# Kernel tuning notes

Hardware: AMD Instinct MI355X
Metric: run time of the kernel (lower is better)

## Reference

```python
import jax, jax.numpy as jnp
import numpy as np

DT = 0.05
TAU = 0.15
SIGMA = float(np.sqrt(2.0 * DT / TAU))  # GaussianNoise default sigma
NOISE_SCALE = 1.0

N = 2048        # nneurons
RANK = 64       # nbg
BATCH = 2048
IN_DIM = 128    # input_sources['stim'] size


def setup_inputs() -> dict:
    key = jax.random.key(0)
    ks = jax.random.split(key, 10)
    inv_sqrt_n = 1.0 / np.sqrt(N)
    return {
        "r_thalamic": jax.random.uniform(ks[0], (BATCH, RANK), jnp.float32),
        "stim": jax.random.normal(ks[1], (BATCH, IN_DIM), jnp.float32),
        "x": jax.random.normal(ks[2], (BATCH, N), jnp.float32) * inv_sqrt_n,
        "r": jax.nn.softplus(jax.random.normal(ks[3], (BATCH, N), jnp.float32) * inv_sqrt_n),
        "J": jax.random.normal(ks[4], (N, N), jnp.float32) * (1.2 * inv_sqrt_n),
        "B": jax.random.normal(ks[5], (1, N), jnp.float32),
        "U": jax.random.normal(ks[6], (N, RANK), jnp.float32) * inv_sqrt_n,
        "V": jax.random.normal(ks[7], (RANK, N), jnp.float32) * inv_sqrt_n,
        "I_stim": jax.random.normal(ks[8], (IN_DIM, N), jnp.float32) * inv_sqrt_n,
        "eps": jax.random.normal(ks[9], (BATCH, N), jnp.float32),
    }


def reference(r_thalamic, stim, x, r, J, B, U, V, I_stim, eps):
    # external input: stim @ I['stim']  -> (batch, N)
    ext = stim @ I_stim
    # bg_tensor @ r == U @ diag(r_thalamic) @ V @ r, computed in low-rank form:
    # (batch, rank) * (batch, rank) -> project back with U
    rec_input = (r_thalamic * (r @ V.T)) @ U.T          # (batch, N)
    pre = -x + r @ J + rec_input + B + ext               # (batch, N)
    noisy = pre + (SIGMA * NOISE_SCALE) * eps            # GaussianNoise
    x_new = x + (DT / TAU) * noisy
    r_new = jax.nn.softplus(x_new)
    return (x_new, r_new)
```

## Files before the change

### kernel.cpp

```cpp
#include <hip/hip_runtime.h>
#include <cstdint>
#include <cstddef>


#define KA 2176
#define KB 2240
#define NN 2048

using frag_ab = __attribute__((ext_vector_type(8))) short;
using frag_cd = __attribute__((ext_vector_type(4))) float;

__device__ __forceinline__ unsigned short f2bf(float f) {
  union { float f; unsigned int i; } v;
  v.f = f;
  unsigned int r = v.i + 0x7fffu + ((v.i >> 16) & 1u);
  return (unsigned short)(r >> 16);
}

__device__ __forceinline__ uint4 cvt8(const float* __restrict__ p) {
  float4 a = *(const float4*)p;
  float4 b = *(const float4*)(p + 4);
  union { uint4 v; unsigned short u[8]; } d;
  d.u[0] = f2bf(a.x); d.u[1] = f2bf(a.y); d.u[2] = f2bf(a.z); d.u[3] = f2bf(a.w);
  d.u[4] = f2bf(b.x); d.u[5] = f2bf(b.y); d.u[6] = f2bf(b.z); d.u[7] = f2bf(b.w);
  return d.v;
}

__device__ __forceinline__ void gl_lds16(const void* g, void* l) {
  __builtin_amdgcn_global_load_lds(
      (const __attribute__((address_space(1))) void*)g,
      (__attribute__((address_space(3))) void*)l, 16, 0, 0);
}

__global__ __launch_bounds__(256) void prep(
    const float* __restrict__ J, const float* __restrict__ Ist,
    const float* __restrict__ rg, const float* __restrict__ stim,
    const float* __restrict__ U, const float* __restrict__ V,
    unsigned short* __restrict__ Ap, unsigned short* __restrict__ Bp,
    float* __restrict__ part) {
  __shared__ unsigned short tile[64 * 66];
  __shared__ alignas(16) unsigned short Ats[32 * 64];
  __shared__ alignas(16) unsigned short Bts[64 * 64];
  const int blk = blockIdx.x;
  const int t = threadIdx.x;

  if (blk < 1088) {
    const float* src;
    int dst_off, cx, cy;
    if (blk < 1024) { src = J;   dst_off = 0;    cx = blk & 31; cy = blk >> 5; }
    else            { src = Ist; dst_off = 2048; cx = (blk - 1024) & 31; cy = (blk - 1024) >> 5; }
    const int r0 = cy * 64, c0 = cx * 64;
    const int sr = t >> 3, c8 = t & 7;
#pragma unroll
    for (int p = 0; p < 2; ++p) {
      const int row = sr + 32 * p;
      union { uint4 v; unsigned short u[8]; } d;
      d.v = cvt8(&src[(size_t)(r0 + row) * 2048 + c0 + c8 * 8]);
#pragma unroll
      for (int e = 0; e < 8; ++e) tile[row * 66 + c8 * 8 + e] = d.u[e];
    }
    __syncthreads();
#pragma unroll
    for (int p = 0; p < 2; ++p) {
      const int scol = sr + 32 * p;
      union { uint4 v; unsigned short u[8]; } d;
#pragma unroll
      for (int e = 0; e < 8; ++e) d.u[e] = tile[(c8 * 8 + e) * 66 + scol];
      *(uint4*)&Bp[(size_t)(c0 + scol) * KB + dst_off + r0 + c8 * 8] = d.v;
    }
  } else if (blk < 3136) {
    const int row = blk - 1088;
    *(uint4*)&Ap[(size_t)row * KA + t * 8] = cvt8(&rg[(size_t)row * 2048 + t * 8]);
    if (t < 24) {
      const int c = 256 + t;
      if (c < 272)
        *(uint4*)&Ap[(size_t)row * KA + c * 8] =
            cvt8(&stim[(size_t)row * 128 + (c - 256) * 8]);
      else
        *(uint4*)&Bp[(size_t)row * KB + c * 8] =
            cvt8(&U[(size_t)row * 64 + (c - 272) * 8]);
    }
  } else {
    const int tb = blk - 3136;
    const int mt = tb & 63, s = tb >> 6;
    const int b0 = mt * 32;
    const int wave = t >> 6, lane = t & 63;
    const int q = lane >> 4, l15 = lane & 15;
    const int arow = t >> 3, ac8 = t & 7;

    const float* gA  = rg + (size_t)(b0 + arow) * 2048 + s * 512 + ac8 * 8;
    const float* gB0 = V  + (size_t)arow        * 2048 + s * 512 + ac8 * 8;
    const float* gB1 = V  + (size_t)(arow + 32) * 2048 + s * 512 + ac8 * 8;

    frag_cd acc0 = {0.f, 0.f, 0.f, 0.f};
    frag_cd acc1 = {0.f, 0.f, 0.f, 0.f};

    for (int kt = 0; kt < 8; ++kt) {
      const int k0 = kt * 64;
      uint4 va  = cvt8(gA + k0);
      uint4 vb0 = cvt8(gB0 + k0);
      uint4 vb1 = cvt8(gB1 + k0);
      __syncthreads();
      *(uint4*)&Ats[t * 8]        = va;
      *(uint4*)&Bts[t * 8]        = vb0;
      *(uint4*)&Bts[2048 + t * 8] = vb1;
      __syncthreads();
#pragma unroll
      for (int ks = 0; ks < 2; ++ks) {
        frag_ab a0 = *(const frag_ab*)&Ats[(l15)      * 64 + ks * 32 + q * 8];
        frag_ab a1 = *(const frag_ab*)&Ats[(16 + l15) * 64 + ks * 32 + q * 8];
        frag_ab b  = *(const frag_ab*)&Bts[(wave * 16 + l15) * 64 + ks * 32 + q * 8];
        acc0 = __builtin_amdgcn_mfma_f32_16x16x32_bf16(a0, b, acc0, 0, 0, 0);
        acc1 = __builtin_amdgcn_mfma_f32_16x16x32_bf16(a1, b, acc1, 0, 0, 0);
      }
    }
    const int p = wave * 16 + l15;
#pragma unroll
    for (int reg = 0; reg < 4; ++reg) {
      const int m0 = q * 4 + reg;
      part[((size_t)s * 2048 + b0 + m0) * 64 + p]      = acc0[reg];
      part[((size_t)s * 2048 + b0 + m0 + 16) * 64 + p] = acc1[reg];
    }
  }
}

__global__ __launch_bounds__(256, 4) void main_gemm(
    const unsigned short* __restrict__ Ap, const unsigned short* __restrict__ Bp,
    const float* __restrict__ part, const float* __restrict__ tha,
    const float* __restrict__ xg, const float* __restrict__ epsg,
    const float* __restrict__ Bvec,
    float* __restrict__ outx, float* __restrict__ outr) {
  __shared__ alignas(16) unsigned short As[64 * 64];
  __shared__ alignas(16) unsigned short Bs[64 * 64];

  const int t = threadIdx.x;
  const int wave = t >> 6, lane = t & 63;
  const int q = lane >> 4, l15 = lane & 15, l7 = lane & 7;
  const int wm = (wave & 1) * 32, wn = (wave >> 1) * 32;
  const int bm0 = blockIdx.y * 64, bn0 = blockIdx.x * 64;

  const unsigned short* gA[2];
  const unsigned short* gB[2];
  unsigned short* lA[2];
  unsigned short* lB[2];
  uint4 tval[2];
#pragma unroll
  for (int r = 0; r < 2; ++r) {
    const int ci = r * 256 + t;
    const int row = ci >> 3;
    const int lc = (ci & 7) ^ (row & 7);
    gA[r] = Ap + (size_t)(bm0 + row) * KA + lc * 8;
    gB[r] = Bp + (size_t)(bn0 + row) * KB + lc * 8;
    lA[r] = As + (size_t)(r * 256 + wave * 64) * 8;
    lB[r] = Bs + (size_t)(r * 256 + wave * 64) * 8;

    const int p0 = lc * 8;
    const size_t base = ((size_t)(bm0 + row)) * 64 + p0;
    float4 s0 = *(const float4*)&part[base];
    float4 s1 = *(const float4*)&part[base + 4];
#pragma unroll
    for (int s = 1; s < 4; ++s) {
      float4 a = *(const float4*)&part[(size_t)s * 131072 + base];
      float4 b = *(const float4*)&part[(size_t)s * 131072 + base + 4];
      s0.x += a.x; s0.y += a.y; s0.z += a.z; s0.w += a.w;
      s1.x += b.x; s1.y += b.y; s1.z += b.z; s1.w += b.w;
    }
    float4 th0 = *(const float4*)&tha[base];
    float4 th1 = *(const float4*)&tha[base + 4];
    union { uint4 v; unsigned short u[8]; } d;
    d.u[0] = f2bf(th0.x * s0.x); d.u[1] = f2bf(th0.y * s0.y);
    d.u[2] = f2bf(th0.z * s0.z); d.u[3] = f2bf(th0.w * s0.w);
    d.u[4] = f2bf(th1.x * s1.x); d.u[5] = f2bf(th1.y * s1.y);
    d.u[6] = f2bf(th1.z * s1.z); d.u[7] = f2bf(th1.w * s1.w);
    tval[r] = d.v;
  }

  frag_cd acc[2][2];
#pragma unroll
  for (int i = 0; i < 2; ++i)
#pragma unroll
    for (int j = 0; j < 2; ++j) {
      frag_cd z = {0.f, 0.f, 0.f, 0.f};
      acc[i][j] = z;
    }

#pragma unroll 1
  for (int kt = 0; kt < 34; ++kt) {
    const int k0 = kt * 64;
    __syncthreads();
#pragma unroll
    for (int r = 0; r < 2; ++r) {
      gl_lds16(gA[r] + k0, lA[r]);
      gl_lds16(gB[r] + k0, lB[r]);
    }
    __syncthreads();
#pragma unroll
    for (int ks = 0; ks < 2; ++ks) {
      const int lc = ks * 4 + q;
      frag_ab af[2], bfr[2];
#pragma unroll
      for (int i = 0; i < 2; ++i) {
        af[i]  = *(const frag_ab*)&As[(wm + i * 16 + l15) * 64 + ((lc ^ l7) * 8)];
        bfr[i] = *(const frag_ab*)&Bs[(wn + i * 16 + l15) * 64 + ((lc ^ l7) * 8)];
      }
#pragma unroll
      for (int i = 0; i < 2; ++i)
#pragma unroll
        for (int j = 0; j < 2; ++j)
          acc[i][j] = __builtin_amdgcn_mfma_f32_16x16x32_bf16(af[i], bfr[j], acc[i][j], 0, 0, 0);
    }
  }

  {
    const int k0 = 34 * 64;
    __syncthreads();
#pragma unroll
    for (int r = 0; r < 2; ++r) {
      *(uint4*)&As[(size_t)(r * 256 + t) * 8] = tval[r];
      gl_lds16(gB[r] + k0, lB[r]);
    }
    __syncthreads();
#pragma unroll
    for (int ks = 0; ks < 2; ++ks) {
      const int lc = ks * 4 + q;
      frag_ab af[2], bfr[2];
#pragma unroll
      for (int i = 0; i < 2; ++i) {
        af[i]  = *(const frag_ab*)&As[(wm + i * 16 + l15) * 64 + ((lc ^ l7) * 8)];
        bfr[i] = *(const frag_ab*)&Bs[(wn + i * 16 + l15) * 64 + ((lc ^ l7) * 8)];
      }
#pragma unroll
      for (int i = 0; i < 2; ++i)
#pragma unroll
        for (int j = 0; j < 2; ++j)
          acc[i][j] = __builtin_amdgcn_mfma_f32_16x16x32_bf16(af[i], bfr[j], acc[i][j], 0, 0, 0);
    }
  }

  const float A_DT = 0.33333334f;
  const float SIG  = 0.81649658092772615f;
#pragma unroll
  for (int j = 0; j < 2; ++j) {
    const int nc = bn0 + wn + j * 16 + l15;
    const float bvf = Bvec[nc];
#pragma unroll
    for (int i = 0; i < 2; ++i) {
#pragma unroll
      for (int reg = 0; reg < 4; ++reg) {
        const int mr = bm0 + wm + i * 16 + q * 4 + reg;
        const size_t off = (size_t)mr * NN + nc;
        const float xf = xg[off];
        const float ef = epsg[off];
        const float xn = xf + A_DT * (acc[i][j][reg] + bvf - xf + SIG * ef);
        outx[off] = xn;
        outr[off] = (xn > 20.f) ? xn : log1pf(__expf(xn));
      }
    }
  }
}

extern "C" void kernel_launch(void* const* d_in, const int* in_sizes, int n_in,
                              void* d_out, int out_size, void* d_ws, size_t ws_size,
                              hipStream_t stream) {
  (void)in_sizes; (void)n_in; (void)out_size; (void)ws_size;
  const float* tha  = (const float*)d_in[0];
  const float* stim = (const float*)d_in[1];
  const float* x    = (const float*)d_in[2];
  const float* r    = (const float*)d_in[3];
  const float* J    = (const float*)d_in[4];
  const float* Bv   = (const float*)d_in[5];
  const float* U    = (const float*)d_in[6];
  const float* V    = (const float*)d_in[7];
  const float* Ist  = (const float*)d_in[8];
  const float* eps  = (const float*)d_in[9];

  unsigned short* Apk = (unsigned short*)d_ws;
  unsigned short* Bpk = Apk + (size_t)NN * KA;
  float* part = (float*)(Bpk + (size_t)NN * KB);
  float* outx = (float*)d_out;
  float* outr = outx + (size_t)NN * NN;

  prep<<<3392, 256, 0, stream>>>(J, Ist, r, stim, U, V, Apk, Bpk, part);
  main_gemm<<<dim3(32, 32), 256, 0, stream>>>(Apk, Bpk, part, tha, x, eps, Bv,
                                              outx, outr);
}
```

Baseline: 180.4 us.

## Enlarge main GEMM tile to 128x64 and remap blocks for XCD locality

The main GEMM block tile grows from 64x64 to 128x64, so each wave computes a 64x32 sub-tile (4x2 MFMA accumulators). This raises MFMA work per LDS B-fragment load and halves the number of blocks. A 1D grid of 512 blocks is remapped so that blocks scheduled on the same XCD share A and B tiles for better L2 reuse. In exchange, registers and LDS per block rise (launch bounds drop to 2 blocks per SIMD), which lowers occupancy and leaves fewer blocks to fill the 256 CUs.

```diff
diff --git a/kernel.cpp b/kernel.cpp
--- a/kernel.cpp
+++ b/kernel.cpp
@@ -124,35 +124,38 @@
   }
 }
 
-__global__ __launch_bounds__(256, 4) void main_gemm(
+__global__ __launch_bounds__(256, 2) void main_gemm(
     const unsigned short* __restrict__ Ap, const unsigned short* __restrict__ Bp,
     const float* __restrict__ part, const float* __restrict__ tha,
     const float* __restrict__ xg, const float* __restrict__ epsg,
     const float* __restrict__ Bvec,
     float* __restrict__ outx, float* __restrict__ outr) {
-  __shared__ alignas(16) unsigned short As[64 * 64];
+  __shared__ alignas(16) unsigned short As[128 * 64];
   __shared__ alignas(16) unsigned short Bs[64 * 64];
 
   const int t = threadIdx.x;
   const int wave = t >> 6, lane = t & 63;
   const int q = lane >> 4, l15 = lane & 15, l7 = lane & 7;
-  const int wm = (wave & 1) * 32, wn = (wave >> 1) * 32;
-  const int bm0 = blockIdx.y * 64, bn0 = blockIdx.x * 64;
-
-  const unsigned short* gA[2];
+  const int wm = (wave & 1) * 64, wn = (wave >> 1) * 32;
+
+  const int bid = blockIdx.x;
+  const int xcd = bid & 7, idx = bid >> 3;
+  const int mt = ((xcd >> 2) << 3) + (idx >> 3);
+  const int nt = ((xcd & 3) << 3) + (idx & 7);
+  const int bm0 = mt * 128, bn0 = nt * 64;
+
+  const unsigned short* gA[4];
   const unsigned short* gB[2];
-  unsigned short* lA[2];
+  unsigned short* lA[4];
   unsigned short* lB[2];
-  uint4 tval[2];
-#pragma unroll
-  for (int r = 0; r < 2; ++r) {
+  uint4 tval[4];
+#pragma unroll
+  for (int r = 0; r < 4; ++r) {
     const int ci = r * 256 + t;
     const int row = ci >> 3;
     const int lc = (ci & 7) ^ (row & 7);
     gA[r] = Ap + (size_t)(bm0 + row) * KA + lc * 8;
-    gB[r] = Bp + (size_t)(bn0 + row) * KB + lc * 8;
     lA[r] = As + (size_t)(r * 256 + wave * 64) * 8;
-    lB[r] = Bs + (size_t)(r * 256 + wave * 64) * 8;
 
     const int p0 = lc * 8;
     const size_t base = ((size_t)(bm0 + row)) * 64 + p0;
@@ -174,10 +177,18 @@
     d.u[6] = f2bf(th1.z * s1.z); d.u[7] = f2bf(th1.w * s1.w);
     tval[r] = d.v;
   }
-
-  frag_cd acc[2][2];
-#pragma unroll
-  for (int i = 0; i < 2; ++i)
+#pragma unroll
+  for (int r = 0; r < 2; ++r) {
+    const int ci = r * 256 + t;
+    const int row = ci >> 3;
+    const int lc = (ci & 7) ^ (row & 7);
+    gB[r] = Bp + (size_t)(bn0 + row) * KB + lc * 8;
+    lB[r] = Bs + (size_t)(r * 256 + wave * 64) * 8;
+  }
+
+  frag_cd acc[4][2];
+#pragma unroll
+  for (int i = 0; i < 4; ++i)
 #pragma unroll
     for (int j = 0; j < 2; ++j) {
       frag_cd z = {0.f, 0.f, 0.f, 0.f};
@@ -189,22 +200,22 @@
     const int k0 = kt * 64;
     __syncthreads();
 #pragma unroll
-    for (int r = 0; r < 2; ++r) {
-      gl_lds16(gA[r] + k0, lA[r]);
-      gl_lds16(gB[r] + k0, lB[r]);
-    }
+    for (int r = 0; r < 4; ++r) gl_lds16(gA[r] + k0, lA[r]);
+#pragma unroll
+    for (int r = 0; r < 2; ++r) gl_lds16(gB[r] + k0, lB[r]);
     __syncthreads();
 #pragma unroll
     for (int ks = 0; ks < 2; ++ks) {
       const int lc = ks * 4 + q;
-      frag_ab af[2], bfr[2];
-#pragma unroll
-      for (int i = 0; i < 2; ++i) {
+      frag_ab af[4], bfr[2];
+#pragma unroll
+      for (int i = 0; i < 4; ++i)
         af[i]  = *(const frag_ab*)&As[(wm + i * 16 + l15) * 64 + ((lc ^ l7) * 8)];
-        bfr[i] = *(const frag_ab*)&Bs[(wn + i * 16 + l15) * 64 + ((lc ^ l7) * 8)];
-      }
-#pragma unroll
-      for (int i = 0; i < 2; ++i)
+#pragma unroll
+      for (int j = 0; j < 2; ++j)
+        bfr[j] = *(const frag_ab*)&Bs[(wn + j * 16 + l15) * 64 + ((lc ^ l7) * 8)];
+#pragma unroll
+      for (int i = 0; i < 4; ++i)
 #pragma unroll
         for (int j = 0; j < 2; ++j)
           acc[i][j] = __builtin_amdgcn_mfma_f32_16x16x32_bf16(af[i], bfr[j], acc[i][j], 0, 0, 0);
@@ -215,22 +226,23 @@
     const int k0 = 34 * 64;
     __syncthreads();
 #pragma unroll
-    for (int r = 0; r < 2; ++r) {
+    for (int r = 0; r < 4; ++r)
       *(uint4*)&As[(size_t)(r * 256 + t) * 8] = tval[r];
-      gl_lds16(gB[r] + k0, lB[r]);
-    }
+#pragma unroll
+    for (int r = 0; r < 2; ++r) gl_lds16(gB[r] + k0, lB[r]);
     __syncthreads();
 #pragma unroll
     for (int ks = 0; ks < 2; ++ks) {
       const int lc = ks * 4 + q;
-      frag_ab af[2], bfr[2];
-#pragma unroll
-      for (int i = 0; i < 2; ++i) {
+      frag_ab af[4], bfr[2];
+#pragma unroll
+      for (int i = 0; i < 4; ++i)
         af[i]  = *(const frag_ab*)&As[(wm + i * 16 + l15) * 64 + ((lc ^ l7) * 8)];
-        bfr[i] = *(const frag_ab*)&Bs[(wn + i * 16 + l15) * 64 + ((lc ^ l7) * 8)];
-      }
-#pragma unroll
-      for (int i = 0; i < 2; ++i)
+#pragma unroll
+      for (int j = 0; j < 2; ++j)
+        bfr[j] = *(const frag_ab*)&Bs[(wn + j * 16 + l15) * 64 + ((lc ^ l7) * 8)];
+#pragma unroll
+      for (int i = 0; i < 4; ++i)
 #pragma unroll
         for (int j = 0; j < 2; ++j)
           acc[i][j] = __builtin_amdgcn_mfma_f32_16x16x32_bf16(af[i], bfr[j], acc[i][j], 0, 0, 0);
@@ -244,7 +256,7 @@
     const int nc = bn0 + wn + j * 16 + l15;
     const float bvf = Bvec[nc];
 #pragma unroll
-    for (int i = 0; i < 2; ++i) {
+    for (int i = 0; i < 4; ++i) {
 #pragma unroll
       for (int reg = 0; reg < 4; ++reg) {
         const int mr = bm0 + wm + i * 16 + q * 4 + reg;
@@ -281,6 +293,6 @@
   float* outr = outx + (size_t)NN * NN;
 
   prep<<<3392, 256, 0, stream>>>(J, Ist, r, stim, U, V, Apk, Bpk, part);
-  main_gemm<<<dim3(32, 32), 256, 0, stream>>>(Apk, Bpk, part, tha, x, eps, Bv,
-                                              outx, outr);
-}
+  main_gemm<<<512, 256, 0, stream>>>(Apk, Bpk, part, tha, x, eps, Bv,
+                                     outx, outr);
+}
```

Result: slower. 191.5 us (+6.1%).

## Double-buffer LDS tiles with async prefetch and remap blocks per XCD

Applied to the files above, without the earlier changes.

The main GEMM now double-buffers the A/B shared-memory tiles and issues the global-to-LDS loads for the next K tile before computing the current one. This replaces two full __syncthreads per iteration with explicit waitcnt and barrier pairs, aiming to hide global load latency behind MFMA work. The grid is also flattened to 1D and remapped so each XCD handles a contiguous 16x8 tile region, which should improve L2 reuse. The cost is twice the LDS per block, which may reduce occupancy. The hand-written vmcnt counts and the final-tile handling are fragile if the load counts change.

```diff
diff --git a/kernel.cpp b/kernel.cpp
--- a/kernel.cpp
+++ b/kernel.cpp
@@ -130,19 +130,22 @@
     const float* __restrict__ xg, const float* __restrict__ epsg,
     const float* __restrict__ Bvec,
     float* __restrict__ outx, float* __restrict__ outr) {
-  __shared__ alignas(16) unsigned short As[64 * 64];
-  __shared__ alignas(16) unsigned short Bs[64 * 64];
+  __shared__ alignas(16) unsigned short As[2][64 * 64];
+  __shared__ alignas(16) unsigned short Bs[2][64 * 64];
 
   const int t = threadIdx.x;
   const int wave = t >> 6, lane = t & 63;
   const int q = lane >> 4, l15 = lane & 15, l7 = lane & 7;
   const int wm = (wave & 1) * 32, wn = (wave >> 1) * 32;
-  const int bm0 = blockIdx.y * 64, bn0 = blockIdx.x * 64;
+
+  const int bid = blockIdx.x;
+  const int xcd = bid & 7, idx = bid >> 3;
+  const int mt = ((xcd >> 2) << 4) + (idx >> 3);
+  const int nt = ((xcd & 3) << 3) + (idx & 7);
+  const int bm0 = mt * 64, bn0 = nt * 64;
 
   const unsigned short* gA[2];
   const unsigned short* gB[2];
-  unsigned short* lA[2];
-  unsigned short* lB[2];
   uint4 tval[2];
 #pragma unroll
   for (int r = 0; r < 2; ++r) {
@@ -151,8 +154,6 @@
     const int lc = (ci & 7) ^ (row & 7);
     gA[r] = Ap + (size_t)(bm0 + row) * KA + lc * 8;
     gB[r] = Bp + (size_t)(bn0 + row) * KB + lc * 8;
-    lA[r] = As + (size_t)(r * 256 + wave * 64) * 8;
-    lB[r] = Bs + (size_t)(r * 256 + wave * 64) * 8;
 
     const int p0 = lc * 8;
     const size_t base = ((size_t)(bm0 + row)) * 64 + p0;
@@ -184,24 +185,51 @@
       acc[i][j] = z;
     }
 
+  asm volatile("s_waitcnt vmcnt(0)" ::: "memory");
+#pragma unroll
+  for (int r = 0; r < 2; ++r) {
+    gl_lds16(gA[r], &As[0][(size_t)(r * 256 + wave * 64) * 8]);
+    gl_lds16(gB[r], &Bs[0][(size_t)(r * 256 + wave * 64) * 8]);
+  }
+
 #pragma unroll 1
   for (int kt = 0; kt < 34; ++kt) {
-    const int k0 = kt * 64;
-    __syncthreads();
-#pragma unroll
-    for (int r = 0; r < 2; ++r) {
-      gl_lds16(gA[r] + k0, lA[r]);
-      gl_lds16(gB[r] + k0, lB[r]);
-    }
-    __syncthreads();
+    const int cur = kt & 1;
+    asm volatile("s_waitcnt lgkmcnt(0)" ::: "memory");
+    __builtin_amdgcn_s_barrier();
+    __builtin_amdgcn_sched_barrier(0);
+    if (kt < 33) {
+      const int k0n = (kt + 1) * 64;
+      unsigned short* dA = &As[cur ^ 1][0];
+      unsigned short* dB = &Bs[cur ^ 1][0];
+#pragma unroll
+      for (int r = 0; r < 2; ++r) {
+        gl_lds16(gA[r] + k0n, dA + (size_t)(r * 256 + wave * 64) * 8);
+        gl_lds16(gB[r] + k0n, dB + (size_t)(r * 256 + wave * 64) * 8);
+      }
+      asm volatile("s_waitcnt vmcnt(4)" ::: "memory");
+    } else {
+      unsigned short* dA = &As[cur ^ 1][0];
+      unsigned short* dB = &Bs[cur ^ 1][0];
+#pragma unroll
+      for (int r = 0; r < 2; ++r) {
+        *(uint4*)&dA[(size_t)(r * 256 + t) * 8] = tval[r];
+        gl_lds16(gB[r] + 34 * 64, dB + (size_t)(r * 256 + wave * 64) * 8);
+      }
+      asm volatile("s_waitcnt vmcnt(2) lgkmcnt(0)" ::: "memory");
+    }
+    __builtin_amdgcn_s_barrier();
+    __builtin_amdgcn_sched_barrier(0);
+    const unsigned short* cA = &As[cur][0];
+    const unsigned short* cB = &Bs[cur][0];
 #pragma unroll
     for (int ks = 0; ks < 2; ++ks) {
       const int lc = ks * 4 + q;
       frag_ab af[2], bfr[2];
 #pragma unroll
       for (int i = 0; i < 2; ++i) {
-        af[i]  = *(const frag_ab*)&As[(wm + i * 16 + l15) * 64 + ((lc ^ l7) * 8)];
-        bfr[i] = *(const frag_ab*)&Bs[(wn + i * 16 + l15) * 64 + ((lc ^ l7) * 8)];
+        af[i]  = *(const frag_ab*)&cA[(wm + i * 16 + l15) * 64 + ((lc ^ l7) * 8)];
+        bfr[i] = *(const frag_ab*)&cB[(wn + i * 16 + l15) * 64 + ((lc ^ l7) * 8)];
       }
 #pragma unroll
       for (int i = 0; i < 2; ++i)
@@ -212,22 +240,19 @@
   }
 
   {
-    const int k0 = 34 * 64;
-    __syncthreads();
-#pragma unroll
-    for (int r = 0; r < 2; ++r) {
-      *(uint4*)&As[(size_t)(r * 256 + t) * 8] = tval[r];
-      gl_lds16(gB[r] + k0, lB[r]);
-    }
-    __syncthreads();
+    asm volatile("s_waitcnt vmcnt(0) lgkmcnt(0)" ::: "memory");
+    __builtin_amdgcn_s_barrier();
+    __builtin_amdgcn_sched_barrier(0);
+    const unsigned short* cA = &As[0][0];
+    const unsigned short* cB = &Bs[0][0];
 #pragma unroll
     for (int ks = 0; ks < 2; ++ks) {
       const int lc = ks * 4 + q;
       frag_ab af[2], bfr[2];
 #pragma unroll
       for (int i = 0; i < 2; ++i) {
-        af[i]  = *(const frag_ab*)&As[(wm + i * 16 + l15) * 64 + ((lc ^ l7) * 8)];
-        bfr[i] = *(const frag_ab*)&Bs[(wn + i * 16 + l15) * 64 + ((lc ^ l7) * 8)];
+        af[i]  = *(const frag_ab*)&cA[(wm + i * 16 + l15) * 64 + ((lc ^ l7) * 8)];
+        bfr[i] = *(const frag_ab*)&cB[(wn + i * 16 + l15) * 64 + ((lc ^ l7) * 8)];
       }
 #pragma unroll
       for (int i = 0; i < 2; ++i)
@@ -281,6 +306,6 @@
   float* outr = outx + (size_t)NN * NN;
 
   prep<<<3392, 256, 0, stream>>>(J, Ist, r, stim, U, V, Apk, Bpk, part);
-  main_gemm<<<dim3(32, 32), 256, 0, stream>>>(Apk, Bpk, part, tha, x, eps, Bv,
-                                              outx, outr);
-}
+  main_gemm<<<1024, 256, 0, stream>>>(Apk, Bpk, part, tha, x, eps, Bv,
+                                      outx, outr);
+}
```

Result: no change. 179.8 us (-0.4%).
